# Performance work log

Hardware: AMD Instinct MI355X
Metric: run time of the kernel (lower is better)

The kernel has to match this reference:

```python
import jax, jax.numpy as jnp
import numpy as np
from jax import lax

# 8-neighbor zero-pad offsets as (left, right, top, bottom), matching nn.ZeroPad2d args
PADS = [(0, 2, 0, 2), (1, 1, 0, 2), (2, 0, 0, 2), (0, 2, 1, 1),
        (2, 0, 1, 1), (0, 2, 2, 0), (1, 1, 2, 0), (2, 0, 2, 0)]
BN_EPS = 1e-5


def conv2d(x, w, pad):
    return lax.conv_general_dilated(x, w, (1, 1), [(pad, pad), (pad, pad)],
                                    dimension_numbers=('NCHW', 'OIHW', 'NCHW'))


def batchnorm(x, gamma, beta, mean, var):
    inv = gamma * lax.rsqrt(var + BN_EPS)
    return x * inv[None, :, None, None] + (beta - mean * inv)[None, :, None, None]


def resize_bilinear(x, oh, ow):
    # F.interpolate(mode='bilinear', align_corners=False)
    n, c, h, w = x.shape
    ys = jnp.clip((jnp.arange(oh, dtype=x.dtype) + 0.5) * (h / oh) - 0.5, 0.0, None)
    xs = jnp.clip((jnp.arange(ow, dtype=x.dtype) + 0.5) * (w / ow) - 0.5, 0.0, None)
    y0 = jnp.floor(ys); x0 = jnp.floor(xs)
    wy = (ys - y0)[:, None]; wx = (xs - x0)[None, :]
    y0i = jnp.clip(y0.astype(jnp.int32), 0, h - 1)
    y1i = jnp.clip(y0i + 1, 0, h - 1)
    x0i = jnp.clip(x0.astype(jnp.int32), 0, w - 1)
    x1i = jnp.clip(x0i + 1, 0, w - 1)
    r0 = x[:, :, y0i, :]; r1 = x[:, :, y1i, :]
    top = r0[:, :, :, x0i] * (1 - wx) + r0[:, :, :, x1i] * wx
    bot = r1[:, :, :, x0i] * (1 - wx) + r1[:, :, :, x1i] * wx
    return top * (1 - wy) + bot * wy


def lrwarp_error(left, disp, right):
    # Warp right image toward left using horizontal disparity (bilinear,
    # zero padding outside), then per-channel absolute photometric error.
    n, c, h, w = right.shape
    xs = jnp.arange(w, dtype=disp.dtype)[None, None, None, :] - disp  # [n,1,h,w]
    x0 = jnp.floor(xs)
    frac = xs - x0
    x0i = x0.astype(jnp.int32)
    x1i = x0i + 1
    v0 = ((x0i >= 0) & (x0i < w)).astype(right.dtype)
    v1 = ((x1i >= 0) & (x1i < w)).astype(right.dtype)
    x0c = jnp.broadcast_to(jnp.clip(x0i, 0, w - 1), (n, c, h, w))
    x1c = jnp.broadcast_to(jnp.clip(x1i, 0, w - 1), (n, c, h, w))
    g0 = jnp.take_along_axis(right, x0c, axis=3) * v0
    g1 = jnp.take_along_axis(right, x1c, axis=3) * v1
    warped = g0 * (1 - frac) + g1 * frac
    return jnp.abs(left - warped)


def setup_inputs() -> dict:
    key = jax.random.key(0)
    ks = jax.random.split(key, 16)
    N, H, W = 8, 256, 256
    inp = {
        'normal_estimation': jax.random.normal(ks[0], (N, 3, H, W), jnp.float32),
        'left_image': jax.random.uniform(ks[1], (N, 3, 512, 512), jnp.float32),
        'right_image': jax.random.uniform(ks[2], (N, 3, 512, 512), jnp.float32),
        'coarse_disparity': jax.random.uniform(ks[3], (N, 1, H, W), jnp.float32),
        'w1': jax.random.normal(ks[4], (32, 12, 3, 3), jnp.float32) * 0.1,
        'g1': jnp.ones((32,), jnp.float32), 'b1': jnp.zeros((32,), jnp.float32),
        'm1': jax.random.normal(ks[5], (32,), jnp.float32) * 0.01,
        'v1': jax.random.uniform(ks[6], (32,), jnp.float32, 0.5, 1.5),
        'w2': jax.random.normal(ks[7], (64, 32, 3, 3), jnp.float32) * 0.1,
        'g2': jnp.ones((64,), jnp.float32), 'b2': jnp.zeros((64,), jnp.float32),
        'm2': jax.random.normal(ks[8], (64,), jnp.float32) * 0.01,
        'v2': jax.random.uniform(ks[9], (64,), jnp.float32, 0.5, 1.5),
        'w3': jax.random.normal(ks[10], (8, 64, 1, 1), jnp.float32) * 0.1,
    }
    return inp


def _forward(normal_estimation, left_image, right_image, coarse_disparity,
             w1, g1, b1, m1, v1, w2, g2, b2, m2, v2, w3):
    H, W = coarse_disparity.shape[-2], coarse_disparity.shape[-1]
    cur_l = resize_bilinear(left_image, H, W)
    cur_r = resize_bilinear(right_image, H, W)
    disp_err = lrwarp_error(cur_l, coarse_disparity, cur_r)
    feats = jnp.concatenate([normal_estimation, cur_l, cur_r, disp_err], axis=1)
    x = jax.nn.relu(batchnorm(conv2d(feats, w1, 1), g1, b1, m1, v1))
    x = jax.nn.relu(batchnorm(conv2d(x, w2, 1), g2, b2, m2, v2))
    aff = jax.nn.relu(conv2d(x, w3, 0))  # [N,8,H,W]
    gate_p = jnp.stack([jnp.pad(aff[:, k], ((0, 0), (t, b), (l, r)))
                        for k, (l, r, t, b) in enumerate(PADS)], axis=1)
    d = coarse_disparity[:, 0]
    disp_p = jnp.stack([jnp.pad(d, ((0, 0), (t, b), (l, r)))
                        for (l, r, t, b) in PADS], axis=1)
    gate = jax.nn.softmax(gate_p, axis=1)
    prop = jnp.sum(gate * disp_p, axis=1, keepdims=True)[:, :, 1:-1, 1:-1]
    return prop * 0.3 + coarse_disparity * 0.7


def reference(normal_estimation, left_image, right_image, coarse_disparity,
              w1, g1, b1, m1, v1, w2, g2, b2, m2, v2, w3):
    return _forward(normal_estimation, left_image, right_image, coarse_disparity,
                    w1, g1, b1, m1, v1, w2, g2, b2, m2, v2, w3)
```

## Files before the change

kernel.cpp:

```cpp
#include <hip/hip_runtime.h>
#include <math.h>

#define NB 8
#define HH 256
#define WW 256
#define HW (HH*WW)

#define OFF_AFFB  0UL
#define OFF_W1FB  8388608UL
#define OFF_B1FB  8400896UL
#define OFF_W2FB  8401024UL
#define OFF_B2FB  8437888UL
#define OFF_W3FB  8438144UL

typedef short  short8 __attribute__((ext_vector_type(8)));
typedef ushort u16x8  __attribute__((ext_vector_type(8)));
typedef ushort u16x4  __attribute__((ext_vector_type(4)));
typedef float  f32x4  __attribute__((ext_vector_type(4)));

__device__ __forceinline__ ushort f2bf(float x) {
  uint u = __float_as_uint(x);
  return (ushort)((u + 0x7FFFu + ((u >> 16) & 1u)) >> 16);
}
__device__ __forceinline__ float bf2f(ushort h) {
  uint u = ((uint)h) << 16;
  return __uint_as_float(u);
}
__device__ __forceinline__ uint pk2bf(float a, float b) {
  uint r;
  asm("v_cvt_pk_bf16_f32 %0, %1, %2" : "=v"(r) : "v"(a), "v"(b));
  return r;
}

__global__ __launch_bounds__(256) void prep_kernel(
    const float* __restrict__ w1, const float* __restrict__ g1,
    const float* __restrict__ b1, const float* __restrict__ m1,
    const float* __restrict__ v1,
    const float* __restrict__ w2, const float* __restrict__ g2,
    const float* __restrict__ b2, const float* __restrict__ m2,
    const float* __restrict__ v2, const float* __restrict__ w3,
    char* __restrict__ wsb) {
  int idx = blockIdx.x * 256 + threadIdx.x;
  ushort* w1f = (ushort*)(wsb + OFF_W1FB);
  float* b1f  = (float*)(wsb + OFF_B1FB);
  ushort* w2f = (ushort*)(wsb + OFF_W2FB);
  float* b2f  = (float*)(wsb + OFF_B2FB);
  ushort* w3f = (ushort*)(wsb + OFF_W3FB);
  if (idx < 6144) {
    int jj = idx & 7;
    int lane = (idx >> 3) & 63;
    int nt = (idx >> 9) & 1;
    int s = idx >> 10;
    int ky = s >> 1, t = s & 1;
    int q = lane >> 4, lx = lane & 15;
    int k = q * 8 + jj;
    int dcol = k >> 4, ch = k & 15;
    int kx = t * 2 + dcol;
    int out = nt * 16 + lx;
    float inv = g1[out] / sqrtf(v1[out] + 1e-5f);
    float val = (ch < 12 && kx < 3) ? w1[((out * 12 + ch) * 3 + ky) * 3 + kx] * inv : 0.f;
    w1f[idx] = f2bf(val);
  }
  int j = idx - 6144;
  if (j >= 0 && j < 18432) {
    int kk   = j >> 11;
    int nt   = (j >> 9) & 3;
    int lane = (j >> 3) & 63;
    int jj   = j & 7;
    int q  = lane >> 4, lx = lane & 15;
    int cs = q * 8 + jj;
    int cin = ((cs & 1) << 4) | (cs >> 1);
    int out = nt * 16 + lx;
    float inv = g2[out] / sqrtf(v2[out] + 1e-5f);
    w2f[j] = f2bf(w2[(out * 32 + cin) * 9 + kk] * inv);
    if (kk == 0 && q == 0 && jj == 0) b2f[out] = b2[out] - m2[out] * inv;
  }
  int k2 = idx - 24576;
  if (k2 >= 0 && k2 < 32) {
    float inv = g1[k2] / sqrtf(v1[k2] + 1e-5f);
    b1f[k2] = b1[k2] - m1[k2] * inv;
  }
  int k3 = idx - 24608;
  if (k3 >= 0 && k3 < 1024) {
    int jj = k3 & 7;
    int lane = (k3 >> 3) & 63;
    int slice = k3 >> 9;
    int q = lane >> 4, lx = lane & 15;
    int cs = slice * 32 + q * 8 + jj;
    int chp = ((cs & 3) << 4) | (cs >> 2);
    w3f[k3] = (lx < 8) ? f2bf(w3[lx * 64 + chp]) : (ushort)0;
  }
}

__global__ __launch_bounds__(256) void trunk_kernel(
    const float* __restrict__ normal, const float* __restrict__ left,
    const float* __restrict__ right, const float* __restrict__ disp,
    char* __restrict__ wsb) {
  __shared__ ushort buf[18304];
  ushort* x1t = buf + 6464;
  uint*   x1u = (uint*)x1t;
  float*  curRt = (float*)x1t;
  const short8* __restrict__ w1fv = (const short8*)(wsb + OFF_W1FB);
  const float* __restrict__ b1f = (const float*)(wsb + OFF_B1FB);
  const short8* __restrict__ w2fv = (const short8*)(wsb + OFF_W2FB);
  const float* __restrict__ b2f = (const float*)(wsb + OFF_B2FB);
  const short8* __restrict__ w3fv = (const short8*)(wsb + OFF_W3FB);
  ushort* aff = (ushort*)(wsb + OFF_AFFB);

  int blk = blockIdx.x;
  int n = blk >> 8;
  int t = blk & 255;
  int ty0 = (t >> 4) << 4;
  int tx0 = (t & 15) << 4;
  int tid = threadIdx.x;
  int lane = tid & 63;
  int wid = tid >> 6;
  int q = lane >> 4;
  int lx = lane & 15;
  bool border = (ty0 == 0) || (ty0 == 240) || (tx0 == 0) || (tx0 == 240);

  for (int p = tid; p < 440; p += 256) {
    int row = p / 22;
    int col = p - row * 22;
    int gyc = min(max(ty0 + row - 2, 0), HH - 1);
    int gxc = min(max(tx0 + col - 3, 0), WW - 1);
#pragma unroll
    for (int c = 0; c < 3; ++c) {
      const float* Rp = right + ((size_t)(n * 3 + c) * 512 + (gyc << 1)) * 512 + (gxc << 1);
      float2 b0 = *(const float2*)Rp;
      float2 b1v = *(const float2*)(Rp + 512);
      curRt[(c * 20 + row) * 24 + col] = 0.25f * (b0.x + b0.y + b1v.x + b1v.y);
    }
  }
  if (tid < 8) *(u16x8*)&buf[(800 + tid) * 8] = (u16x8)0;
  __syncthreads();

  for (int p = tid; p < 400; p += 256) {
    int row = p / 20;
    int col = p - row * 20;
    int gy = ty0 + row - 2, gx = tx0 + col - 2;
    uint pk[8];
    bool ib = ((unsigned)gy < 256u) && ((unsigned)gx < 256u);
    if (ib) {
      float tv[12];
#pragma unroll
      for (int c = 0; c < 3; ++c) {
        const float* Lp = left + ((size_t)(n * 3 + c) * 512 + (gy << 1)) * 512 + (gx << 1);
        float2 a0 = *(const float2*)Lp;
        float2 a1 = *(const float2*)(Lp + 512);
        tv[3 + c] = 0.25f * (a0.x + a0.y + a1.x + a1.y);
        tv[c] = normal[(size_t)(n * 3 + c) * HW + gy * WW + gx];
        tv[6 + c] = curRt[(c * 20 + row) * 24 + col + 1];
      }
      float d = disp[(size_t)n * HW + gy * WW + gx];
      float xs = (float)gx - d;
      float x0f = floorf(xs);
      float fr = xs - x0f;
      int ix0 = (int)x0f;
      int ix1 = ix0 + 1;
      float vm0 = ((unsigned)ix0 < 256u) ? 1.f : 0.f;
      float vm1 = ((unsigned)ix1 < 256u) ? 1.f : 0.f;
      int l0 = min(max(min(max(ix0, 0), WW - 1) - tx0 + 3, 0), 23);
      int l1 = min(max(min(max(ix1, 0), WW - 1) - tx0 + 3, 0), 23);
#pragma unroll
      for (int c = 0; c < 3; ++c) {
        float wv = curRt[(c * 20 + row) * 24 + l0] * vm0 * (1.f - fr)
                 + curRt[(c * 20 + row) * 24 + l1] * vm1 * fr;
        tv[9 + c] = fabsf(tv[3 + c] - wv);
      }
#pragma unroll
      for (int k = 0; k < 6; ++k) pk[k] = pk2bf(tv[2 * k], tv[2 * k + 1]);
      pk[6] = 0u; pk[7] = 0u;
    } else {
#pragma unroll
      for (int k = 0; k < 8; ++k) pk[k] = 0u;
    }
    int e0 = 2 * p;
    int e1 = 2 * p + 1;
    int s0 = e0 ^ ((e0 >> 3) & 7);
    int s1 = e1 ^ ((e1 >> 3) & 7);
    *(uint4*)&buf[s0 * 8] = make_uint4(pk[0], pk[1], pk[2], pk[3]);
    *(uint4*)&buf[s1 * 8] = make_uint4(pk[4], pk[5], pk[6], pk[7]);
  }
  __syncthreads();

  {
    short8 bw1[6][2];
#pragma unroll
    for (int s = 0; s < 6; ++s)
#pragma unroll
      for (int nt = 0; nt < 2; ++nt) bw1[s][nt] = w1fv[(s * 2 + nt) * 64 + lane];
    float bias1[2] = {b1f[lx], b1f[16 + lx]};
    int laneoff = (lx << 1) + ((q >> 1) << 1) + (q & 1);
    int colbT = 32 + ((lx & 1) << 1) + ((q >> 1) << 1) + (q & 1);
    int rowT = lx >> 1;
    for (int m = wid; m < 21; m += 4) {
      f32x4 a1[2];
      a1[0] = (f32x4)0.f;
      a1[1] = (f32x4)0.f;
      int tb = m - 18;
      int Gb;
      if (m < 18) Gb = m * 40 + laneoff;
      else        Gb = min(tb * 8 + rowT, 17) * 40 + colbT;
#pragma unroll
      for (int s = 0; s < 6; ++s) {
        int G = Gb + (s >> 1) * 40 + (s & 1) * 4;
        int slot = G ^ ((G >> 3) & 7);
        short8 a = *(const short8*)&buf[slot * 8];
        a1[0] = __builtin_amdgcn_mfma_f32_16x16x32_bf16(a, bw1[s][0], a1[0], 0, 0, 0);
        a1[1] = __builtin_amdgcn_mfma_f32_16x16x32_bf16(a, bw1[s][1], a1[1], 0, 0, 0);
      }
      if (m < 18) {
        int base = (m * 18 + (q << 2)) * 18 + lx;
        if (!border) {
#pragma unroll
          for (int r = 0; r < 4; ++r) {
            float v0 = fmaxf(a1[0][r] + bias1[0], 0.f);
            float v1 = fmaxf(a1[1][r] + bias1[1], 0.f);
            x1u[base + r * 18] = pk2bf(v0, v1);
          }
        } else {
          bool gyok = (unsigned)(ty0 + m - 1) < 256u;
          int gx0 = tx0 - 1 + (q << 2);
#pragma unroll
          for (int r = 0; r < 4; ++r) {
            bool ok = gyok && ((unsigned)(gx0 + r) < 256u);
            float v0 = ok ? fmaxf(a1[0][r] + bias1[0], 0.f) : 0.f;
            float v1 = ok ? fmaxf(a1[1][r] + bias1[1], 0.f) : 0.f;
            x1u[base + r * 18] = pk2bf(v0, v1);
          }
        }
      } else {
#pragma unroll
        for (int r = 0; r < 4; ++r) {
          int io = (q << 2) + r;
          int hy = tb * 8 + (io >> 1);
          int hx = 16 + (io & 1);
          if (hy < 18) {
            float v0 = fmaxf(a1[0][r] + bias1[0], 0.f);
            float v1 = fmaxf(a1[1][r] + bias1[1], 0.f);
            if (border) {
              bool ok = ((unsigned)(ty0 + hy - 1) < 256u) && ((unsigned)(tx0 + hx - 1) < 256u);
              v0 = ok ? v0 : 0.f;
              v1 = ok ? v1 : 0.f;
            }
            x1u[(hy * 18 + hx) * 18 + lx] = pk2bf(v0, v1);
          }
        }
      }
    }
  }
  __syncthreads();

  f32x4 acc[4][4];
#pragma unroll
  for (int mt = 0; mt < 4; ++mt)
#pragma unroll
    for (int nt = 0; nt < 4; ++nt) acc[mt][nt] = (f32x4)0.f;
#pragma unroll
  for (int kk = 0; kk < 9; ++kk) {
    int ky = kk / 3, kx = kk - ky * 3;
    short8 a[4], b[4];
#pragma unroll
    for (int mt = 0; mt < 4; ++mt) {
      int row = wid * 4 + mt;
      a[mt] = *(const short8*)&x1t[((row + ky) * 18 + lx + kx) * 36 + q * 8];
    }
#pragma unroll
    for (int nt = 0; nt < 4; ++nt) b[nt] = w2fv[(kk * 4 + nt) * 64 + lane];
#pragma unroll
    for (int mt = 0; mt < 4; ++mt)
#pragma unroll
      for (int nt = 0; nt < 4; ++nt)
        acc[mt][nt] = __builtin_amdgcn_mfma_f32_16x16x32_bf16(a[mt], b[nt], acc[mt][nt], 0, 0, 0);
  }
  float bias2q[4] = {b2f[lx], b2f[16 + lx], b2f[32 + lx], b2f[48 + lx]};
  __syncthreads();

#pragma unroll
  for (int mt = 0; mt < 4; ++mt) {
    int row = wid * 4 + mt;
#pragma unroll
    for (int r = 0; r < 4; ++r) {
      int p = row * 16 + (q << 2) + r;
      float c0 = fmaxf(acc[mt][0][r] + bias2q[0], 0.f);
      float c1 = fmaxf(acc[mt][1][r] + bias2q[1], 0.f);
      float c2 = fmaxf(acc[mt][2][r] + bias2q[2], 0.f);
      float c3 = fmaxf(acc[mt][3][r] + bias2q[3], 0.f);
      uint2 pv;
      pv.x = pk2bf(c0, c1);
      pv.y = pk2bf(c2, c3);
      *(uint2*)&buf[p * 70 + (lx << 2)] = pv;
    }
  }
  __syncthreads();

  short8 bw3[2];
  bw3[0] = w3fv[lane];
  bw3[1] = w3fv[64 + lane];
  f32x4 acc3[4];
#pragma unroll
  for (int mt = 0; mt < 4; ++mt) acc3[mt] = (f32x4)0.f;
#pragma unroll
  for (int mt = 0; mt < 4; ++mt) {
    int p = wid * 64 + mt * 16 + lx;
#pragma unroll
    for (int s = 0; s < 2; ++s) {
      short8 a3 = *(const short8*)&buf[p * 70 + s * 32 + q * 8];
      acc3[mt] = __builtin_amdgcn_mfma_f32_16x16x32_bf16(a3, bw3[s], acc3[mt], 0, 0, 0);
    }
  }
  __syncthreads();
  if (lx < 8) {
#pragma unroll
    for (int mt = 0; mt < 4; ++mt) {
#pragma unroll
      for (int r = 0; r < 4; ++r) {
        int pix = (wid * 4 + mt) * 16 + (q << 2) + r;
        buf[pix * 8 + lx] = f2bf(fmaxf(acc3[mt][r], 0.f));
      }
    }
  }
  __syncthreads();
  {
    int py = ty0 + (tid >> 4);
    int px = tx0 + (tid & 15);
    u16x8 v = *(const u16x8*)&buf[tid * 8];
    *(u16x8*)&aff[((size_t)n * HW + (size_t)py * WW + px) * 8] = v;
  }
}

__global__ __launch_bounds__(256) void final_kernel(const float* __restrict__ disp,
                                                    const char* __restrict__ wsb,
                                                    float* __restrict__ out) {
  int gid = blockIdx.x * 256 + threadIdx.x;
  int n = gid >> 15;
  int r = gid & 32767;
  int i = r >> 7;
  int j0 = (r & 127) << 1;
  const ushort* affi = (const ushort*)(wsb + OFF_AFFB);
  float d4[3][4];
  u16x8 A[3][4];
#pragma unroll
  for (int rr = 0; rr < 3; ++rr) {
    int yc = min(max(i + rr - 1, 0), HH - 1);
    const float* dp = disp + (size_t)n * HW + yc * WW;
    float2 c2 = *(const float2*)(dp + j0);
    d4[rr][1] = c2.x; d4[rr][2] = c2.y;
    d4[rr][0] = dp[max(j0 - 1, 0)];
    d4[rr][3] = dp[min(j0 + 2, WW - 1)];
    const ushort* ap = affi + ((size_t)n * HW + (size_t)yc * WW) * 8;
    A[rr][0] = *(const u16x8*)(ap + (size_t)max(j0 - 1, 0) * 8);
    A[rr][1] = *(const u16x8*)(ap + (size_t)j0 * 8);
    A[rr][2] = *(const u16x8*)(ap + (size_t)(j0 + 1) * 8);
    A[rr][3] = *(const u16x8*)(ap + (size_t)min(j0 + 2, WW - 1) * 8);
  }
  const int dy[8] = {1, 1, 1, 0, 0, -1, -1, -1};
  const int dx[8] = {1, 0, -1, 1, -1, 1, 0, -1};
  bool vup = (i > 0), vdn = (i < HH - 1);
  float2 res;
#pragma unroll
  for (int p = 0; p < 2; ++p) {
    float g[8], dv[8];
#pragma unroll
    for (int k = 0; k < 8; ++k) {
      int rr = dy[k] + 1;
      int cc = p + 1 + dx[k];
      bool vy = (rr == 1) ? true : ((rr == 2) ? vdn : vup);
      bool ok = vy && ((unsigned)(j0 + p + dx[k]) < (unsigned)WW);
      g[k] = ok ? bf2f(A[rr][cc][k]) : 0.f;
      dv[k] = ok ? d4[rr][cc] : 0.f;
    }
    float m = g[0];
#pragma unroll
    for (int k = 1; k < 8; ++k) m = fmaxf(m, g[k]);
    float se = 0.f, sed = 0.f;
#pragma unroll
    for (int k = 0; k < 8; ++k) {
      float e = __expf(g[k] - m);
      se += e;
      sed += e * dv[k];
    }
    (&res.x)[p] = 0.3f * (sed / se) + 0.7f * d4[1][p + 1];
  }
  *(float2*)(out + (size_t)n * HW + i * WW + j0) = res;
}

extern "C" void kernel_launch(void* const* d_in, const int* in_sizes, int n_in,
                              void* d_out, int out_size, void* d_ws, size_t ws_size,
                              hipStream_t stream) {
  const float* normal = (const float*)d_in[0];
  const float* left   = (const float*)d_in[1];
  const float* right  = (const float*)d_in[2];
  const float* disp   = (const float*)d_in[3];
  const float* w1 = (const float*)d_in[4];
  const float* g1 = (const float*)d_in[5];
  const float* b1 = (const float*)d_in[6];
  const float* m1 = (const float*)d_in[7];
  const float* v1 = (const float*)d_in[8];
  const float* w2 = (const float*)d_in[9];
  const float* g2 = (const float*)d_in[10];
  const float* b2 = (const float*)d_in[11];
  const float* m2 = (const float*)d_in[12];
  const float* v2 = (const float*)d_in[13];
  const float* w3 = (const float*)d_in[14];
  char* wsb  = (char*)d_ws;
  float* out = (float*)d_out;

  hipLaunchKernelGGL(prep_kernel, dim3(101), dim3(256), 0, stream,
                     w1, g1, b1, m1, v1, w2, g2, b2, m2, v2, w3, wsb);
  hipLaunchKernelGGL(trunk_kernel, dim3(2048), dim3(256), 0, stream,
                     normal, left, right, disp, wsb);
  hipLaunchKernelGGL(final_kernel, dim3(1024), dim3(256), 0, stream, disp, wsb, out);
}
```

Measured before the change: 170.2 us.

## Fuse propagation softmax into trunk kernel with halo recompute; precompute downsampled images

Removes the separate final kernel and the global affinity buffer. The trunk kernel now computes conv outputs over a halo-extended 18x18 region, keeps the affinities and disparities in shared memory, and does the 8-neighbor softmax propagation in place. Downsampling of the left and right images moves into the prep kernel, which writes them to the workspace so the trunk reads them directly instead of averaging 2x2 blocks from the full-resolution inputs. In exchange, conv1, conv2 and conv3 are redone on the halo pixels, shared memory use rises, and the extra pre-kernel pass adds memory traffic.

After: 203.0 us. +19.2%, slower.

```diff
diff --git a/kernel.cpp b/kernel.cpp
--- a/kernel.cpp
+++ b/kernel.cpp
@@ -1,21 +1,20 @@
 #include <hip/hip_runtime.h>
 #include <math.h>
 
-#define NB 8
 #define HH 256
 #define WW 256
 #define HW (HH*WW)
 
-#define OFF_AFFB  0UL
-#define OFF_W1FB  8388608UL
-#define OFF_B1FB  8400896UL
-#define OFF_W2FB  8401024UL
-#define OFF_B2FB  8437888UL
-#define OFF_W3FB  8438144UL
+#define OFF_CURL  0UL
+#define OFF_CURR  6291456UL
+#define OFF_W1FB  12582912UL
+#define OFF_B1FB  12595200UL
+#define OFF_W2FB  12595328UL
+#define OFF_B2FB  12632192UL
+#define OFF_W3FB  12632448UL
 
 typedef short  short8 __attribute__((ext_vector_type(8)));
 typedef ushort u16x8  __attribute__((ext_vector_type(8)));
-typedef ushort u16x4  __attribute__((ext_vector_type(4)));
 typedef float  f32x4  __attribute__((ext_vector_type(4)));
 
 __device__ __forceinline__ ushort f2bf(float x) {
@@ -32,7 +31,8 @@
   return r;
 }
 
-__global__ __launch_bounds__(256) void prep_kernel(
+__global__ __launch_bounds__(256) void pre_kernel(
+    const float* __restrict__ left, const float* __restrict__ right,
     const float* __restrict__ w1, const float* __restrict__ g1,
     const float* __restrict__ b1, const float* __restrict__ m1,
     const float* __restrict__ v1,
@@ -40,7 +40,26 @@
     const float* __restrict__ b2, const float* __restrict__ m2,
     const float* __restrict__ v2, const float* __restrict__ w3,
     char* __restrict__ wsb) {
-  int idx = blockIdx.x * 256 + threadIdx.x;
+  int blk = blockIdx.x;
+  if (blk < 6144) {
+    int idx = blk * 256 + threadIdx.x;
+    int pid = idx >> 15;
+    int within = idx & 32767;
+    int y = within >> 7;
+    int x0 = (within & 127) << 1;
+    const float* src = (pid < 24) ? left : right;
+    int pp = (pid < 24) ? pid : pid - 24;
+    float* dst = (float*)(wsb + ((pid < 24) ? OFF_CURL : OFF_CURR)) + (size_t)pp * HW;
+    const float* s0 = src + ((size_t)pp * 512 + (y << 1)) * 512 + (x0 << 1);
+    float4 a0 = *(const float4*)s0;
+    float4 a1 = *(const float4*)(s0 + 512);
+    float2 o;
+    o.x = 0.25f * (a0.x + a0.y + a1.x + a1.y);
+    o.y = 0.25f * (a0.z + a0.w + a1.z + a1.w);
+    *(float2*)(dst + y * WW + x0) = o;
+    return;
+  }
+  int idx = (blk - 6144) * 256 + threadIdx.x;
   ushort* w1f = (ushort*)(wsb + OFF_W1FB);
   float* b1f  = (float*)(wsb + OFF_B1FB);
   ushort* w2f = (ushort*)(wsb + OFF_W2FB);
@@ -93,19 +112,20 @@
 }
 
 __global__ __launch_bounds__(256) void trunk_kernel(
-    const float* __restrict__ normal, const float* __restrict__ left,
-    const float* __restrict__ right, const float* __restrict__ disp,
-    char* __restrict__ wsb) {
-  __shared__ ushort buf[18304];
-  ushort* x1t = buf + 6464;
+    const float* __restrict__ normal, const float* __restrict__ disp,
+    char* __restrict__ wsb, float* __restrict__ out) {
+  __shared__ __align__(16) ushort buf[25812];
+  ushort* x1t = buf + 7808;
   uint*   x1u = (uint*)x1t;
-  float*  curRt = (float*)x1t;
+  ushort* affT = buf + 22208;
+  float*  dispT = (float*)(buf + 24800);
   const short8* __restrict__ w1fv = (const short8*)(wsb + OFF_W1FB);
   const float* __restrict__ b1f = (const float*)(wsb + OFF_B1FB);
   const short8* __restrict__ w2fv = (const short8*)(wsb + OFF_W2FB);
   const float* __restrict__ b2f = (const float*)(wsb + OFF_B2FB);
   const short8* __restrict__ w3fv = (const short8*)(wsb + OFF_W3FB);
-  ushort* aff = (ushort*)(wsb + OFF_AFFB);
+  const float* __restrict__ curLg = (const float*)(wsb + OFF_CURL);
+  const float* __restrict__ curRg = (const float*)(wsb + OFF_CURR);
 
   int blk = blockIdx.x;
   int n = blk >> 8;
@@ -119,40 +139,28 @@
   int lx = lane & 15;
   bool border = (ty0 == 0) || (ty0 == 240) || (tx0 == 0) || (tx0 == 240);
 
-  for (int p = tid; p < 440; p += 256) {
+  if (tid < 8) {
+    int e = 968 + tid;
+    int s = e ^ ((e >> 3) & 7);
+    *(u16x8*)&buf[s * 8] = (u16x8)0;
+  }
+  for (int p = tid; p < 484; p += 256) {
     int row = p / 22;
     int col = p - row * 22;
-    int gyc = min(max(ty0 + row - 2, 0), HH - 1);
-    int gxc = min(max(tx0 + col - 3, 0), WW - 1);
-#pragma unroll
-    for (int c = 0; c < 3; ++c) {
-      const float* Rp = right + ((size_t)(n * 3 + c) * 512 + (gyc << 1)) * 512 + (gxc << 1);
-      float2 b0 = *(const float2*)Rp;
-      float2 b1v = *(const float2*)(Rp + 512);
-      curRt[(c * 20 + row) * 24 + col] = 0.25f * (b0.x + b0.y + b1v.x + b1v.y);
-    }
-  }
-  if (tid < 8) *(u16x8*)&buf[(800 + tid) * 8] = (u16x8)0;
-  __syncthreads();
-
-  for (int p = tid; p < 400; p += 256) {
-    int row = p / 20;
-    int col = p - row * 20;
-    int gy = ty0 + row - 2, gx = tx0 + col - 2;
+    int gy = ty0 + row - 3, gx = tx0 + col - 3;
     uint pk[8];
-    bool ib = ((unsigned)gy < 256u) && ((unsigned)gx < 256u);
+    float d = 0.f;
+    bool ib = ((unsigned)gy < 256u) & ((unsigned)gx < 256u);
     if (ib) {
+      size_t pix = (size_t)gy * WW + gx;
       float tv[12];
 #pragma unroll
       for (int c = 0; c < 3; ++c) {
-        const float* Lp = left + ((size_t)(n * 3 + c) * 512 + (gy << 1)) * 512 + (gx << 1);
-        float2 a0 = *(const float2*)Lp;
-        float2 a1 = *(const float2*)(Lp + 512);
-        tv[3 + c] = 0.25f * (a0.x + a0.y + a1.x + a1.y);
-        tv[c] = normal[(size_t)(n * 3 + c) * HW + gy * WW + gx];
-        tv[6 + c] = curRt[(c * 20 + row) * 24 + col + 1];
-      }
-      float d = disp[(size_t)n * HW + gy * WW + gx];
+        tv[c]     = normal[(size_t)(n * 3 + c) * HW + pix];
+        tv[3 + c] = curLg[(size_t)(n * 3 + c) * HW + pix];
+        tv[6 + c] = curRg[(size_t)(n * 3 + c) * HW + pix];
+      }
+      d = disp[(size_t)n * HW + pix];
       float xs = (float)gx - d;
       float x0f = floorf(xs);
       float fr = xs - x0f;
@@ -160,12 +168,12 @@
       int ix1 = ix0 + 1;
       float vm0 = ((unsigned)ix0 < 256u) ? 1.f : 0.f;
       float vm1 = ((unsigned)ix1 < 256u) ? 1.f : 0.f;
-      int l0 = min(max(min(max(ix0, 0), WW - 1) - tx0 + 3, 0), 23);
-      int l1 = min(max(min(max(ix1, 0), WW - 1) - tx0 + 3, 0), 23);
+      int x0c = min(max(ix0, 0), WW - 1);
+      int x1c = min(max(ix1, 0), WW - 1);
 #pragma unroll
       for (int c = 0; c < 3; ++c) {
-        float wv = curRt[(c * 20 + row) * 24 + l0] * vm0 * (1.f - fr)
-                 + curRt[(c * 20 + row) * 24 + l1] * vm1 * fr;
+        const float* rp = curRg + (size_t)(n * 3 + c) * HW + (size_t)gy * WW;
+        float wv = rp[x0c] * vm0 * (1.f - fr) + rp[x1c] * vm1 * fr;
         tv[9 + c] = fabsf(tv[3 + c] - wv);
       }
 #pragma unroll
@@ -175,8 +183,8 @@
 #pragma unroll
       for (int k = 0; k < 8; ++k) pk[k] = 0u;
     }
-    int e0 = 2 * p;
-    int e1 = 2 * p + 1;
+    dispT[row * 23 + col] = d;
+    int e0 = 2 * p, e1 = 2 * p + 1;
     int s0 = e0 ^ ((e0 >> 3) & 7);
     int s1 = e1 ^ ((e1 >> 3) & 7);
     *(uint4*)&buf[s0 * 8] = make_uint4(pk[0], pk[1], pk[2], pk[3]);
@@ -187,41 +195,35 @@
   {
     short8 bw1[6][2];
 #pragma unroll
-    for (int s = 0; s < 6; ++s)
-#pragma unroll
-      for (int nt = 0; nt < 2; ++nt) bw1[s][nt] = w1fv[(s * 2 + nt) * 64 + lane];
+    for (int s = 0; s < 6; ++s) {
+      bw1[s][0] = w1fv[(s * 2 + 0) * 64 + lane];
+      bw1[s][1] = w1fv[(s * 2 + 1) * 64 + lane];
+    }
     float bias1[2] = {b1f[lx], b1f[16 + lx]};
     int laneoff = (lx << 1) + ((q >> 1) << 1) + (q & 1);
-    int colbT = 32 + ((lx & 1) << 1) + ((q >> 1) << 1) + (q & 1);
-    int rowT = lx >> 1;
-    for (int m = wid; m < 21; m += 4) {
+    int tailoff = (((lx >> 2) * 22) + 16 + (lx & 3)) * 2 + ((q >> 1) << 1) + (q & 1);
+    for (int m = wid; m < 25; m += 4) {
       f32x4 a1[2];
-      a1[0] = (f32x4)0.f;
-      a1[1] = (f32x4)0.f;
-      int tb = m - 18;
-      int Gb;
-      if (m < 18) Gb = m * 40 + laneoff;
-      else        Gb = min(tb * 8 + rowT, 17) * 40 + colbT;
+      a1[0] = (f32x4)0.f; a1[1] = (f32x4)0.f;
+      int Gb = (m < 20) ? (m * 44 + laneoff) : ((m - 20) * 176 + tailoff);
 #pragma unroll
       for (int s = 0; s < 6; ++s) {
-        int G = Gb + (s >> 1) * 40 + (s & 1) * 4;
+        int G = Gb + (s >> 1) * 44 + (s & 1) * 4;
         int slot = G ^ ((G >> 3) & 7);
         short8 a = *(const short8*)&buf[slot * 8];
         a1[0] = __builtin_amdgcn_mfma_f32_16x16x32_bf16(a, bw1[s][0], a1[0], 0, 0, 0);
         a1[1] = __builtin_amdgcn_mfma_f32_16x16x32_bf16(a, bw1[s][1], a1[1], 0, 0, 0);
       }
-      if (m < 18) {
-        int base = (m * 18 + (q << 2)) * 18 + lx;
+      if (m < 20) {
+        int base = (m * 20 + (q << 2)) * 18 + lx;
         if (!border) {
 #pragma unroll
-          for (int r = 0; r < 4; ++r) {
-            float v0 = fmaxf(a1[0][r] + bias1[0], 0.f);
-            float v1 = fmaxf(a1[1][r] + bias1[1], 0.f);
-            x1u[base + r * 18] = pk2bf(v0, v1);
-          }
+          for (int r = 0; r < 4; ++r)
+            x1u[base + r * 18] = pk2bf(fmaxf(a1[0][r] + bias1[0], 0.f),
+                                       fmaxf(a1[1][r] + bias1[1], 0.f));
         } else {
-          bool gyok = (unsigned)(ty0 + m - 1) < 256u;
-          int gx0 = tx0 - 1 + (q << 2);
+          bool gyok = (unsigned)(ty0 - 2 + m) < 256u;
+          int gx0 = tx0 - 2 + (q << 2);
 #pragma unroll
           for (int r = 0; r < 4; ++r) {
             bool ok = gyok && ((unsigned)(gx0 + r) < 256u);
@@ -231,20 +233,97 @@
           }
         }
       } else {
+        int row = (m - 20) * 4 + q;
+        int base = (row * 20 + 16) * 18 + lx;
+        bool gyok = (unsigned)(ty0 - 2 + row) < 256u;
 #pragma unroll
         for (int r = 0; r < 4; ++r) {
-          int io = (q << 2) + r;
-          int hy = tb * 8 + (io >> 1);
-          int hx = 16 + (io & 1);
-          if (hy < 18) {
-            float v0 = fmaxf(a1[0][r] + bias1[0], 0.f);
-            float v1 = fmaxf(a1[1][r] + bias1[1], 0.f);
-            if (border) {
-              bool ok = ((unsigned)(ty0 + hy - 1) < 256u) && ((unsigned)(tx0 + hx - 1) < 256u);
-              v0 = ok ? v0 : 0.f;
-              v1 = ok ? v1 : 0.f;
+          bool ok = !border || (gyok && ((unsigned)(tx0 + 14 + r) < 256u));
+          float v0 = ok ? fmaxf(a1[0][r] + bias1[0], 0.f) : 0.f;
+          float v1 = ok ? fmaxf(a1[1][r] + bias1[1], 0.f) : 0.f;
+          x1u[base + r * 18] = pk2bf(v0, v1);
+        }
+      }
+    }
+  }
+  __syncthreads();
+
+  {
+    short8 bw3[2];
+    bw3[0] = w3fv[lane];
+    bw3[1] = w3fv[64 + lane];
+    float bias2q[4] = {b2f[lx], b2f[16 + lx], b2f[32 + lx], b2f[48 + lx]};
+    ushort* scr = buf + wid * 1120;
+#pragma unroll
+    for (int it = 0; it < 3; ++it) {
+      int m0 = it * 8 + wid * 2;
+      bool v[2] = {m0 < 21, m0 + 1 < 21};
+      int ar[2], ac[2];
+#pragma unroll
+      for (int u = 0; u < 2; ++u) {
+        int m = m0 + u;
+        if (m < 18) { ar[u] = m; ac[u] = lx; }
+        else { int tb = m - 18; ar[u] = min(tb * 8 + (lx >> 1), 17); ac[u] = 16 + (lx & 1); }
+      }
+      f32x4 acc[2][4];
+#pragma unroll
+      for (int u = 0; u < 2; ++u)
+#pragma unroll
+        for (int nt = 0; nt < 4; ++nt) acc[u][nt] = (f32x4)0.f;
+#pragma unroll
+      for (int kk = 0; kk < 9; ++kk) {
+        int ky = kk / 3, kx = kk - ky * 3;
+        short8 b[4];
+#pragma unroll
+        for (int nt = 0; nt < 4; ++nt) b[nt] = w2fv[(kk * 4 + nt) * 64 + lane];
+#pragma unroll
+        for (int u = 0; u < 2; ++u) {
+          if (v[u]) {
+            short8 a = *(const short8*)&x1t[((ar[u] + ky) * 20 + ac[u] + kx) * 36 + q * 8];
+#pragma unroll
+            for (int nt = 0; nt < 4; ++nt)
+              acc[u][nt] = __builtin_amdgcn_mfma_f32_16x16x32_bf16(a, b[nt], acc[u][nt], 0, 0, 0);
+          }
+        }
+      }
+#pragma unroll
+      for (int u = 0; u < 2; ++u) {
+        int m = m0 + u;
+        if (!v[u]) continue;
+#pragma unroll
+        for (int r = 0; r < 4; ++r) {
+          uint2 pv;
+          pv.x = pk2bf(fmaxf(acc[u][0][r] + bias2q[0], 0.f),
+                       fmaxf(acc[u][1][r] + bias2q[1], 0.f));
+          pv.y = pk2bf(fmaxf(acc[u][2][r] + bias2q[2], 0.f),
+                       fmaxf(acc[u][3][r] + bias2q[3], 0.f));
+          *(uint2*)&scr[((q << 2) + r) * 70 + (lx << 2)] = pv;
+        }
+        asm volatile("s_waitcnt lgkmcnt(0)" ::: "memory");
+        f32x4 a3acc = (f32x4)0.f;
+#pragma unroll
+        for (int s = 0; s < 2; ++s) {
+          short8 a3 = *(const short8*)&scr[lx * 70 + s * 32 + q * 8];
+          a3acc = __builtin_amdgcn_mfma_f32_16x16x32_bf16(a3, bw3[s], a3acc, 0, 0, 0);
+        }
+        if (lx < 8) {
+#pragma unroll
+          for (int r = 0; r < 4; ++r) {
+            int pit = (q << 2) + r;
+            int row, col;
+            bool valid = true;
+            if (m < 18) { row = m; col = pit; }
+            else {
+              int tb = m - 18;
+              int pg = tb * 16 + pit;
+              row = pg >> 1; col = 16 + (pg & 1);
+              valid = (pg < 36);
             }
-            x1u[(hy * 18 + hx) * 18 + lx] = pk2bf(v0, v1);
+            if (valid) {
+              bool ok = !border || (((unsigned)(ty0 - 1 + row) < 256u) &&
+                                    ((unsigned)(tx0 - 1 + col) < 256u));
+              affT[(row * 18 + col) * 8 + lx] = ok ? f2bf(fmaxf(a3acc[r], 0.f)) : (ushort)0;
+            }
           }
         }
       }
@@ -252,124 +331,16 @@
   }
   __syncthreads();
 
-  f32x4 acc[4][4];
-#pragma unroll
-  for (int mt = 0; mt < 4; ++mt)
-#pragma unroll
-    for (int nt = 0; nt < 4; ++nt) acc[mt][nt] = (f32x4)0.f;
-#pragma unroll
-  for (int kk = 0; kk < 9; ++kk) {
-    int ky = kk / 3, kx = kk - ky * 3;
-    short8 a[4], b[4];
-#pragma unroll
-    for (int mt = 0; mt < 4; ++mt) {
-      int row = wid * 4 + mt;
-      a[mt] = *(const short8*)&x1t[((row + ky) * 18 + lx + kx) * 36 + q * 8];
-    }
-#pragma unroll
-    for (int nt = 0; nt < 4; ++nt) b[nt] = w2fv[(kk * 4 + nt) * 64 + lane];
-#pragma unroll
-    for (int mt = 0; mt < 4; ++mt)
-#pragma unroll
-      for (int nt = 0; nt < 4; ++nt)
-        acc[mt][nt] = __builtin_amdgcn_mfma_f32_16x16x32_bf16(a[mt], b[nt], acc[mt][nt], 0, 0, 0);
-  }
-  float bias2q[4] = {b2f[lx], b2f[16 + lx], b2f[32 + lx], b2f[48 + lx]};
-  __syncthreads();
-
-#pragma unroll
-  for (int mt = 0; mt < 4; ++mt) {
-    int row = wid * 4 + mt;
-#pragma unroll
-    for (int r = 0; r < 4; ++r) {
-      int p = row * 16 + (q << 2) + r;
-      float c0 = fmaxf(acc[mt][0][r] + bias2q[0], 0.f);
-      float c1 = fmaxf(acc[mt][1][r] + bias2q[1], 0.f);
-      float c2 = fmaxf(acc[mt][2][r] + bias2q[2], 0.f);
-      float c3 = fmaxf(acc[mt][3][r] + bias2q[3], 0.f);
-      uint2 pv;
-      pv.x = pk2bf(c0, c1);
-      pv.y = pk2bf(c2, c3);
-      *(uint2*)&buf[p * 70 + (lx << 2)] = pv;
-    }
-  }
-  __syncthreads();
-
-  short8 bw3[2];
-  bw3[0] = w3fv[lane];
-  bw3[1] = w3fv[64 + lane];
-  f32x4 acc3[4];
-#pragma unroll
-  for (int mt = 0; mt < 4; ++mt) acc3[mt] = (f32x4)0.f;
-#pragma unroll
-  for (int mt = 0; mt < 4; ++mt) {
-    int p = wid * 64 + mt * 16 + lx;
-#pragma unroll
-    for (int s = 0; s < 2; ++s) {
-      short8 a3 = *(const short8*)&buf[p * 70 + s * 32 + q * 8];
-      acc3[mt] = __builtin_amdgcn_mfma_f32_16x16x32_bf16(a3, bw3[s], acc3[mt], 0, 0, 0);
-    }
-  }
-  __syncthreads();
-  if (lx < 8) {
-#pragma unroll
-    for (int mt = 0; mt < 4; ++mt) {
-#pragma unroll
-      for (int r = 0; r < 4; ++r) {
-        int pix = (wid * 4 + mt) * 16 + (q << 2) + r;
-        buf[pix * 8 + lx] = f2bf(fmaxf(acc3[mt][r], 0.f));
-      }
-    }
-  }
-  __syncthreads();
   {
-    int py = ty0 + (tid >> 4);
-    int px = tx0 + (tid & 15);
-    u16x8 v = *(const u16x8*)&buf[tid * 8];
-    *(u16x8*)&aff[((size_t)n * HW + (size_t)py * WW + px) * 8] = v;
-  }
-}
-
-__global__ __launch_bounds__(256) void final_kernel(const float* __restrict__ disp,
-                                                    const char* __restrict__ wsb,
-                                                    float* __restrict__ out) {
-  int gid = blockIdx.x * 256 + threadIdx.x;
-  int n = gid >> 15;
-  int r = gid & 32767;
-  int i = r >> 7;
-  int j0 = (r & 127) << 1;
-  const ushort* affi = (const ushort*)(wsb + OFF_AFFB);
-  float d4[3][4];
-  u16x8 A[3][4];
-#pragma unroll
-  for (int rr = 0; rr < 3; ++rr) {
-    int yc = min(max(i + rr - 1, 0), HH - 1);
-    const float* dp = disp + (size_t)n * HW + yc * WW;
-    float2 c2 = *(const float2*)(dp + j0);
-    d4[rr][1] = c2.x; d4[rr][2] = c2.y;
-    d4[rr][0] = dp[max(j0 - 1, 0)];
-    d4[rr][3] = dp[min(j0 + 2, WW - 1)];
-    const ushort* ap = affi + ((size_t)n * HW + (size_t)yc * WW) * 8;
-    A[rr][0] = *(const u16x8*)(ap + (size_t)max(j0 - 1, 0) * 8);
-    A[rr][1] = *(const u16x8*)(ap + (size_t)j0 * 8);
-    A[rr][2] = *(const u16x8*)(ap + (size_t)(j0 + 1) * 8);
-    A[rr][3] = *(const u16x8*)(ap + (size_t)min(j0 + 2, WW - 1) * 8);
-  }
-  const int dy[8] = {1, 1, 1, 0, 0, -1, -1, -1};
-  const int dx[8] = {1, 0, -1, 1, -1, 1, 0, -1};
-  bool vup = (i > 0), vdn = (i < HH - 1);
-  float2 res;
-#pragma unroll
-  for (int p = 0; p < 2; ++p) {
+    int py = tid >> 4, px = tid & 15;
+    int r2 = py + 1, c2 = px + 1;
+    const int dy[8] = {1, 1, 1, 0, 0, -1, -1, -1};
+    const int dx[8] = {1, 0, -1, 1, -1, 1, 0, -1};
     float g[8], dv[8];
 #pragma unroll
     for (int k = 0; k < 8; ++k) {
-      int rr = dy[k] + 1;
-      int cc = p + 1 + dx[k];
-      bool vy = (rr == 1) ? true : ((rr == 2) ? vdn : vup);
-      bool ok = vy && ((unsigned)(j0 + p + dx[k]) < (unsigned)WW);
-      g[k] = ok ? bf2f(A[rr][cc][k]) : 0.f;
-      dv[k] = ok ? d4[rr][cc] : 0.f;
+      g[k]  = bf2f(affT[((r2 + dy[k]) * 18 + (c2 + dx[k])) * 8 + k]);
+      dv[k] = dispT[(py + 3 + dy[k]) * 23 + (px + 3 + dx[k])];
     }
     float m = g[0];
 #pragma unroll
@@ -381,9 +352,9 @@
       se += e;
       sed += e * dv[k];
     }
-    (&res.x)[p] = 0.3f * (sed / se) + 0.7f * d4[1][p + 1];
-  }
-  *(float2*)(out + (size_t)n * HW + i * WW + j0) = res;
+    float dc = dispT[(py + 3) * 23 + (px + 3)];
+    out[(size_t)n * HW + (size_t)(ty0 + py) * WW + tx0 + px] = 0.3f * (sed / se) + 0.7f * dc;
+  }
 }
 
 extern "C" void kernel_launch(void* const* d_in, const int* in_sizes, int n_in,
@@ -407,9 +378,8 @@
   char* wsb  = (char*)d_ws;
   float* out = (float*)d_out;
 
-  hipLaunchKernelGGL(prep_kernel, dim3(101), dim3(256), 0, stream,
-                     w1, g1, b1, m1, v1, w2, g2, b2, m2, v2, w3, wsb);
+  hipLaunchKernelGGL(pre_kernel, dim3(6245), dim3(256), 0, stream,
+                     left, right, w1, g1, b1, m1, v1, w2, g2, b2, m2, v2, w3, wsb);
   hipLaunchKernelGGL(trunk_kernel, dim3(2048), dim3(256), 0, stream,
-                     normal, left, right, disp, wsb);
-  hipLaunchKernelGGL(final_kernel, dim3(1024), dim3(256), 0, stream, disp, wsb, out);
-}
+                     normal, disp, wsb, out);
+}
```
